# Optimization experiments

Measured on AMD Instinct MI355X. Metric: run time of the kernel, lower is better.

The kernel has to match this reference:

```python
import jax, jax.numpy as jnp
import numpy as np
import math

D_MODEL = 1024
NUM_HEADS = 16
HEAD_DIM = D_MODEL // NUM_HEADS
BATCH = 2
SEQ = 2048
THETA = 10000.0


def _rope_tables(seq_len, head_dim, theta=THETA):
    inv_freq = 1.0 / theta ** (jnp.arange(0, head_dim, 2, dtype=jnp.float32) / head_dim)
    pos = jnp.arange(seq_len, dtype=jnp.float32)
    freqs = jnp.outer(pos, inv_freq)                 # [S, hd/2]
    emb = jnp.concatenate([freqs, freqs], axis=-1)   # [S, hd]
    return jnp.cos(emb), jnp.sin(emb)


def _rotate_half(x):
    x1, x2 = jnp.split(x, 2, axis=-1)
    return jnp.concatenate([-x2, x1], axis=-1)


def setup_inputs() -> dict:
    key = jax.random.key(0)
    k1, k2, k3 = jax.random.split(key, 3)
    x = jax.random.normal(k1, (BATCH, SEQ, D_MODEL), dtype=jnp.float32)
    # causal mask: 1 where attend allowed, 0 where masked
    mask = jnp.tril(jnp.ones((SEQ, SEQ), dtype=jnp.int32))[None, None]
    w_qkv = jax.random.normal(k2, (D_MODEL, 3 * D_MODEL), dtype=jnp.float32) / math.sqrt(D_MODEL)
    w_out = jax.random.normal(k3, (D_MODEL, D_MODEL), dtype=jnp.float32) / math.sqrt(D_MODEL)
    return {"x": x, "mask": mask, "w_qkv": w_qkv, "w_out": w_out}


def reference(x, mask, w_qkv, w_out):
    B, S, _ = x.shape
    qkv = x @ w_qkv                                          # [B,S,3*D]
    qkv = qkv.reshape(B, S, 3, NUM_HEADS, HEAD_DIM)
    qkv = jnp.transpose(qkv, (2, 0, 3, 1, 4))                # [3,B,H,S,hd]
    q, k, v = qkv[0], qkv[1], qkv[2]
    cos, sin = _rope_tables(S, HEAD_DIM)                     # [S,hd]
    cos = cos[None, None]; sin = sin[None, None]
    q = q * cos + _rotate_half(q) * sin
    k = k * cos + _rotate_half(k) * sin
    scores = jnp.einsum('bhqd,bhkd->bhqk', q, k) / math.sqrt(HEAD_DIM)
    scores = jnp.where(mask == 0, -jnp.inf, scores)
    attn = jax.nn.softmax(scores, axis=-1)                   # dropout p=0 (eval)
    out = jnp.einsum('bhqk,bhkd->bhqd', attn, v)             # [B,H,S,hd]
    out = jnp.transpose(out, (0, 2, 1, 3)).reshape(B, S, D_MODEL)
    return out @ w_out
```

## Files before the change

### kernel.cpp

```cpp
#include <hip/hip_runtime.h>

typedef __bf16 bf16;
typedef __bf16 bf16x4 __attribute__((ext_vector_type(4)));
typedef __bf16 bf16x8 __attribute__((ext_vector_type(8)));
typedef float f32x4 __attribute__((ext_vector_type(4)));

constexpr int BATCH = 2;
constexpr int SEQ   = 2048;
constexpr int DMODEL= 1024;
constexpr int NH    = 16;
constexpr int HD    = 64;
constexpr int M_ROWS= BATCH * SEQ;
constexpr int N_QKV = 3 * DMODEL;

__device__ __forceinline__ void gl_lds16(const bf16* g, bf16* l) {
  __builtin_amdgcn_global_load_lds(
      (const __attribute__((address_space(1))) unsigned int*)g,
      (__attribute__((address_space(3))) unsigned int*)l, 16, 0, 0);
}

__global__ __launch_bounds__(256) void transpose_cast_kernel(
    const float* __restrict__ src, bf16* __restrict__ dst, int R, int C) {
  __shared__ float tile[32][33];
  const int c0 = blockIdx.x * 32, r0 = blockIdx.y * 32;
  const int tx = threadIdx.x, ty = threadIdx.y;
#pragma unroll
  for (int i = 0; i < 4; i++)
    tile[ty + 8 * i][tx] = src[(size_t)(r0 + ty + 8 * i) * C + c0 + tx];
  __syncthreads();
#pragma unroll
  for (int i = 0; i < 4; i++)
    dst[(size_t)(c0 + ty + 8 * i) * R + r0 + tx] = (bf16)tile[tx][ty + 8 * i];
}

__global__ __launch_bounds__(256) void cast_f32_bf16(
    const float* __restrict__ src, bf16* __restrict__ dst) {
  const int i = (blockIdx.x * 256 + threadIdx.x) * 8;
  float4 f0 = *(const float4*)&src[i];
  float4 f1 = *(const float4*)&src[i + 4];
  bf16x8 v;
  v[0] = (bf16)f0.x; v[1] = (bf16)f0.y; v[2] = (bf16)f0.z; v[3] = (bf16)f0.w;
  v[4] = (bf16)f1.x; v[5] = (bf16)f1.y; v[6] = (bf16)f1.z; v[7] = (bf16)f1.w;
  *(bf16x8*)&dst[i] = v;
}

#define GEMM_BODY(A, BT, K)                                                    \
  __shared__ bf16 As[128 * 32];                                                \
  __shared__ bf16 Bs[128 * 32];                                                \
  const int t = threadIdx.x;                                                   \
  const int m0 = blockIdx.y * 128;                                             \
  const int n0 = blockIdx.x * 128;                                             \
  const int w = t >> 6, lane = t & 63, g = lane >> 4, li = lane & 15;          \
  const int r0w = (w & 1) * 64, c0w = (w >> 1) * 64;                           \
  f32x4 acc[4][4] = {};                                                        \
  for (int k0 = 0; k0 < (K); k0 += 32) {                                       \
    __syncthreads();                                                           \
    _Pragma("unroll") for (int c = 0; c < 2; c++) {                            \
      const int idx = (w * 2 + c) * 64 + lane;                                 \
      const int row = idx >> 2, col = (idx & 3) * 8;                           \
      gl_lds16(&(A)[(size_t)(m0 + row) * (K) + k0 + col],                      \
               &As[(w * 2 + c) * 512]);                                        \
      gl_lds16(&(BT)[(size_t)(n0 + row) * (K) + k0 + col],                     \
               &Bs[(w * 2 + c) * 512]);                                        \
    }                                                                          \
    __syncthreads();                                                           \
    bf16x8 a[4], b[4];                                                         \
    _Pragma("unroll") for (int mt = 0; mt < 4; mt++)                           \
        a[mt] = *(const bf16x8*)&As[(r0w + mt * 16 + li) * 32 + g * 8];        \
    _Pragma("unroll") for (int nt = 0; nt < 4; nt++)                           \
        b[nt] = *(const bf16x8*)&Bs[(c0w + nt * 16 + li) * 32 + g * 8];        \
    _Pragma("unroll") for (int mt = 0; mt < 4; mt++)                           \
        _Pragma("unroll") for (int nt = 0; nt < 4; nt++)                       \
            acc[mt][nt] = __builtin_amdgcn_mfma_f32_16x16x32_bf16(             \
                a[mt], b[nt], acc[mt][nt], 0, 0, 0);                           \
  }

__global__ __launch_bounds__(256) void gemm_out(
    const bf16* __restrict__ A, const bf16* __restrict__ BT,
    float* __restrict__ C, int M, int N, int K) {
  GEMM_BODY(A, BT, K)
#pragma unroll
  for (int mt = 0; mt < 4; mt++)
#pragma unroll
    for (int nt = 0; nt < 4; nt++)
#pragma unroll
      for (int r = 0; r < 4; r++) {
        const int m = m0 + r0w + mt * 16 + g * 4 + r;
        const int n = n0 + c0w + nt * 16 + li;
        C[(size_t)m * N + n] = acc[mt][nt][r];
      }
}

__global__ __launch_bounds__(256) void gemm_qkv_rope(
    const bf16* __restrict__ A, const bf16* __restrict__ BT,
    bf16* __restrict__ Qb, bf16* __restrict__ Kb, bf16* __restrict__ Vt) {
  constexpr int K = DMODEL;
  GEMM_BODY(A, BT, K)

  const int region = n0 >> 10;
  const int b = m0 >> 11;
  const int h = ((n0 + c0w) >> 6) & 15;
  const size_t bh = (size_t)(b * NH + h);

  if (region < 2) {
    bf16* dst = region == 0 ? Qb : Kb;
    const float outsc = region == 0 ? 0.125f * 1.44269504f : 1.f;
    const float L = 13.287712379549449f;
    const float if0 = exp2f(-(float)(2 * li) / 64.f * L);
    const float if1 = exp2f(-(float)(2 * (li + 16)) / 64.f * L);
#pragma unroll
    for (int mt = 0; mt < 4; mt++)
#pragma unroll
      for (int r = 0; r < 4; r++) {
        const int s = (m0 + r0w + mt * 16 + g * 4 + r) & (SEQ - 1);
        float cs[2], sn[2];
        __sincosf((float)s * if0, &sn[0], &cs[0]);
        __sincosf((float)s * if1, &sn[1], &cs[1]);
#pragma unroll
        for (int nt = 0; nt < 4; nt++) {
          const int d = nt * 16 + li;
          const int par = nt & 1;
          const float a = acc[mt][nt][r];
          const float ap = acc[mt][nt ^ 2][r];
          const float v = (nt < 2) ? a * cs[par] - ap * sn[par]
                                   : a * cs[par] + ap * sn[par];
          dst[(bh * SEQ + s) * HD + d] = (bf16)(v * outsc);
        }
      }
  } else {
#pragma unroll
    for (int mt = 0; mt < 4; mt++)
#pragma unroll
      for (int nt = 0; nt < 4; nt++) {
        const int s = (m0 + r0w + mt * 16 + g * 4) & (SEQ - 1);
        const int d = nt * 16 + li;
        bf16x4 v;
#pragma unroll
        for (int r = 0; r < 4; r++) v[r] = (bf16)acc[mt][nt][r];
        *(bf16x4*)&Vt[(bh * HD + d) * SEQ + s] = v;
      }
  }
}

__global__ __launch_bounds__(256) void flash_attn4(
    const bf16* __restrict__ Q, const bf16* __restrict__ Kb,
    const bf16* __restrict__ Vt, bf16* __restrict__ Oout) {
  const int f = blockIdx.x;
  const int c = f & 255, half = f >> 8;
  const int bh = c >> 3, idx = c & 7;
  const int qt = half ? 15 - idx : idx;
  const int q0 = qt * 128;
  const int t = threadIdx.x, w = t >> 6, lane = t & 63, g = lane >> 4,
            li = lane & 15;

  __shared__ bf16 Ks[2][4096];
  __shared__ bf16 Vs[2][4096];
  __shared__ bf16 Pl[4][32][72];

  const bf16* Qh = Q  + (size_t)bh * SEQ * HD;
  const bf16* Kh = Kb + (size_t)bh * SEQ * HD;
  const bf16* Vh = Vt + (size_t)bh * HD * SEQ;

  const int qw = q0 + w * 32;

  bf16x8 qf[2][2];
#pragma unroll
  for (int mt = 0; mt < 2; mt++)
#pragma unroll
    for (int ks = 0; ks < 2; ks++)
      qf[mt][ks] =
          *(const bf16x8*)&Qh[(size_t)(qw + mt * 16 + li) * HD + ks * 32 + g * 8];

  f32x4 o[2][4] = {};
  float l_[2][4] = {};

  const int sp0 = (w * 2) * 64 + lane, sp1 = (w * 2 + 1) * 64 + lane;
  const int sr0 = sp0 >> 3, sc0 = ((sp0 & 7) ^ (sr0 & 7)) * 8;
  const int sr1 = sp1 >> 3, sc1 = ((sp1 & 7) ^ (sr1 & 7)) * 8;

  const int jend = q0 + 128;
  gl_lds16(&Kh[(size_t)sr0 * HD + sc0], &Ks[0][(w * 2) * 512]);
  gl_lds16(&Vh[(size_t)sr0 * SEQ + sc0], &Vs[0][(w * 2) * 512]);
  gl_lds16(&Kh[(size_t)sr1 * HD + sc1], &Ks[0][(w * 2 + 1) * 512]);
  gl_lds16(&Vh[(size_t)sr1 * SEQ + sc1], &Vs[0][(w * 2 + 1) * 512]);
  __syncthreads();

  for (int j0 = 0; j0 < jend; j0 += 64) {
    const int cur = (j0 >> 6) & 1, nxt = cur ^ 1;
    if (j0 + 64 < jend) {
      const int jn = j0 + 64;
      gl_lds16(&Kh[(size_t)(jn + sr0) * HD + sc0], &Ks[nxt][(w * 2) * 512]);
      gl_lds16(&Vh[(size_t)sr0 * SEQ + jn + sc0], &Vs[nxt][(w * 2) * 512]);
      gl_lds16(&Kh[(size_t)(jn + sr1) * HD + sc1], &Ks[nxt][(w * 2 + 1) * 512]);
      gl_lds16(&Vh[(size_t)sr1 * SEQ + jn + sc1], &Vs[nxt][(w * 2 + 1) * 512]);
    }

    if (j0 <= qw + 31) {
      f32x4 sacc[2][4] = {};
#pragma unroll
      for (int ks = 0; ks < 2; ks++)
#pragma unroll
        for (int nt = 0; nt < 4; nt++) {
          const int rK = nt * 16 + li;
          const int pK = rK * 8 + ((ks * 4 + g) ^ (li & 7));
          bf16x8 kf = *(const bf16x8*)&Ks[cur][pK * 8];
          sacc[0][nt] = __builtin_amdgcn_mfma_f32_16x16x32_bf16(
              qf[0][ks], kf, sacc[0][nt], 0, 0, 0);
          sacc[1][nt] = __builtin_amdgcn_mfma_f32_16x16x32_bf16(
              qf[1][ks], kf, sacc[1][nt], 0, 0, 0);
        }

      const bool masked = (j0 + 63 > qw);
#pragma unroll
      for (int mt = 0; mt < 2; mt++)
#pragma unroll
        for (int nt = 0; nt < 4; nt++)
#pragma unroll
          for (int r = 0; r < 4; r++) {
            float v = sacc[mt][nt][r];
            if (masked) {
              const int kc = j0 + nt * 16 + li;
              const int qr = qw + mt * 16 + g * 4 + r;
              v = (kc <= qr) ? v : -1e30f;
            }
            const float p = exp2f(v);
            l_[mt][r] += p;
            Pl[w][mt * 16 + g * 4 + r][nt * 16 + li] = (bf16)p;
          }

#pragma unroll
      for (int ks = 0; ks < 2; ks++) {
        bf16x8 pf0 = *(const bf16x8*)&Pl[w][li][ks * 32 + g * 8];
        bf16x8 pf1 = *(const bf16x8*)&Pl[w][16 + li][ks * 32 + g * 8];
#pragma unroll
        for (int dt = 0; dt < 4; dt++) {
          const int rV = dt * 16 + li;
          const int pV = rV * 8 + ((ks * 4 + g) ^ (li & 7));
          bf16x8 vf = *(const bf16x8*)&Vs[cur][pV * 8];
          o[0][dt] = __builtin_amdgcn_mfma_f32_16x16x32_bf16(pf0, vf, o[0][dt],
                                                             0, 0, 0);
          o[1][dt] = __builtin_amdgcn_mfma_f32_16x16x32_bf16(pf1, vf, o[1][dt],
                                                             0, 0, 0);
        }
      }
    }
    __syncthreads();
  }

#pragma unroll
  for (int off = 1; off < 16; off <<= 1)
#pragma unroll
    for (int mt = 0; mt < 2; mt++)
#pragma unroll
      for (int r = 0; r < 4; r++) l_[mt][r] += __shfl_xor(l_[mt][r], off, 64);

  const int b = bh >> 4, h = bh & 15;
#pragma unroll
  for (int mt = 0; mt < 2; mt++)
#pragma unroll
    for (int dt = 0; dt < 4; dt++)
#pragma unroll
      for (int r = 0; r < 4; r++) {
        const int s = qw + mt * 16 + g * 4 + r;
        const int d = dt * 16 + li;
        const float v = o[mt][dt][r] / l_[mt][r];
        Oout[((size_t)(b * SEQ + s)) * DMODEL + h * 64 + d] = (bf16)v;
      }
}

extern "C" void kernel_launch(void* const* d_in, const int* in_sizes, int n_in,
                              void* d_out, int out_size, void* d_ws,
                              size_t ws_size, hipStream_t stream) {
  const float* x     = (const float*)d_in[0];
  const float* w_qkv = (const float*)d_in[2];
  const float* w_out = (const float*)d_in[3];
  float* out = (float*)d_out;

  char* ws = (char*)d_ws;
  bf16* WqkvT = (bf16*)(ws);
  bf16* WoutT = (bf16*)(ws + 6291456);
  bf16* xb    = (bf16*)(ws + 8388608);
  bf16* Qb    = (bf16*)(ws + 16777216);
  bf16* Kbuf  = (bf16*)(ws + 25165824);
  bf16* Vt    = (bf16*)(ws + 33554432);
  bf16* attn  = (bf16*)(ws + 41943040);

  cast_f32_bf16<<<M_ROWS * DMODEL / 2048, 256, 0, stream>>>(x, xb);
  transpose_cast_kernel<<<dim3(N_QKV / 32, DMODEL / 32), dim3(32, 8), 0,
                          stream>>>(w_qkv, WqkvT, DMODEL, N_QKV);
  transpose_cast_kernel<<<dim3(DMODEL / 32, DMODEL / 32), dim3(32, 8), 0,
                          stream>>>(w_out, WoutT, DMODEL, DMODEL);
  gemm_qkv_rope<<<dim3(N_QKV / 128, M_ROWS / 128), 256, 0, stream>>>(
      xb, WqkvT, Qb, Kbuf, Vt);
  flash_attn4<<<dim3(512), 256, 0, stream>>>(Qb, Kbuf, Vt, attn);
  gemm_out<<<dim3(DMODEL / 128, M_ROWS / 128), 256, 0, stream>>>(
      attn, WoutT, out, M_ROWS, DMODEL, DMODEL);
}
```

Measured before the change: 228.6 us.

## Split flash attention across 8 waves with 16-row query tiles and causal tile skipping

The attention kernel now uses 512 threads (8 waves), and each wave owns 16 query rows instead of 32. The cooperative K/V loads become one load per thread per tile instead of two. In diagonal tiles, the QK MFMAs for fully masked 16-column sub-tiles are skipped and their P entries written as zero. The P scratch buffer moves to an XOR-swizzled layout to reduce LDS bank conflicts. This aims to raise wave-level parallelism and cut wasted causal work, at the cost of less Q-fragment reuse per K/V read and more barrier participants per block.

```diff
diff --git a/kernel.cpp b/kernel.cpp
--- a/kernel.cpp
+++ b/kernel.cpp
@@ -142,7 +142,7 @@
   }
 }
 
-__global__ __launch_bounds__(256) void flash_attn4(
+__global__ __launch_bounds__(512, 4) void flash_attn5(
     const bf16* __restrict__ Q, const bf16* __restrict__ Kb,
     const bf16* __restrict__ Vt, bf16* __restrict__ Oout) {
   const int f = blockIdx.x;
@@ -155,94 +155,91 @@
 
   __shared__ bf16 Ks[2][4096];
   __shared__ bf16 Vs[2][4096];
-  __shared__ bf16 Pl[4][32][72];
+  __shared__ bf16 Pl[8 * 1024];
 
   const bf16* Qh = Q  + (size_t)bh * SEQ * HD;
   const bf16* Kh = Kb + (size_t)bh * SEQ * HD;
   const bf16* Vh = Vt + (size_t)bh * HD * SEQ;
 
-  const int qw = q0 + w * 32;
-
-  bf16x8 qf[2][2];
-#pragma unroll
-  for (int mt = 0; mt < 2; mt++)
-#pragma unroll
-    for (int ks = 0; ks < 2; ks++)
-      qf[mt][ks] =
-          *(const bf16x8*)&Qh[(size_t)(qw + mt * 16 + li) * HD + ks * 32 + g * 8];
-
-  f32x4 o[2][4] = {};
-  float l_[2][4] = {};
-
-  const int sp0 = (w * 2) * 64 + lane, sp1 = (w * 2 + 1) * 64 + lane;
-  const int sr0 = sp0 >> 3, sc0 = ((sp0 & 7) ^ (sr0 & 7)) * 8;
-  const int sr1 = sp1 >> 3, sc1 = ((sp1 & 7) ^ (sr1 & 7)) * 8;
+  const int qw = q0 + w * 16;
+
+  bf16x8 qf[2];
+#pragma unroll
+  for (int ks = 0; ks < 2; ks++)
+    qf[ks] = *(const bf16x8*)&Qh[(size_t)(qw + li) * HD + ks * 32 + g * 8];
+
+  f32x4 o[4] = {};
+  float l_[4] = {};
+
+  const int p = w * 64 + lane;
+  const int sr = p >> 3, sc = ((p & 7) ^ (sr & 7)) * 8;
+  const int ldsoff = w * 512;
 
   const int jend = q0 + 128;
-  gl_lds16(&Kh[(size_t)sr0 * HD + sc0], &Ks[0][(w * 2) * 512]);
-  gl_lds16(&Vh[(size_t)sr0 * SEQ + sc0], &Vs[0][(w * 2) * 512]);
-  gl_lds16(&Kh[(size_t)sr1 * HD + sc1], &Ks[0][(w * 2 + 1) * 512]);
-  gl_lds16(&Vh[(size_t)sr1 * SEQ + sc1], &Vs[0][(w * 2 + 1) * 512]);
+  gl_lds16(&Kh[(size_t)sr * HD + sc], &Ks[0][ldsoff]);
+  gl_lds16(&Vh[(size_t)sr * SEQ + sc], &Vs[0][ldsoff]);
   __syncthreads();
 
   for (int j0 = 0; j0 < jend; j0 += 64) {
     const int cur = (j0 >> 6) & 1, nxt = cur ^ 1;
     if (j0 + 64 < jend) {
       const int jn = j0 + 64;
-      gl_lds16(&Kh[(size_t)(jn + sr0) * HD + sc0], &Ks[nxt][(w * 2) * 512]);
-      gl_lds16(&Vh[(size_t)sr0 * SEQ + jn + sc0], &Vs[nxt][(w * 2) * 512]);
-      gl_lds16(&Kh[(size_t)(jn + sr1) * HD + sc1], &Ks[nxt][(w * 2 + 1) * 512]);
-      gl_lds16(&Vh[(size_t)sr1 * SEQ + jn + sc1], &Vs[nxt][(w * 2 + 1) * 512]);
+      gl_lds16(&Kh[(size_t)(jn + sr) * HD + sc], &Ks[nxt][ldsoff]);
+      gl_lds16(&Vh[(size_t)sr * SEQ + jn + sc], &Vs[nxt][ldsoff]);
     }
 
-    if (j0 <= qw + 31) {
-      f32x4 sacc[2][4] = {};
+    if (j0 <= qw + 15) {
+      const bool masked = (j0 + 63 > qw);
+      const int ntlim = masked ? ((qw + 15 - j0) >> 4) + 1 : 4;
+
+      f32x4 sacc[4] = {};
 #pragma unroll
       for (int ks = 0; ks < 2; ks++)
 #pragma unroll
         for (int nt = 0; nt < 4; nt++) {
+          if (nt >= ntlim) continue;
           const int rK = nt * 16 + li;
           const int pK = rK * 8 + ((ks * 4 + g) ^ (li & 7));
           bf16x8 kf = *(const bf16x8*)&Ks[cur][pK * 8];
-          sacc[0][nt] = __builtin_amdgcn_mfma_f32_16x16x32_bf16(
-              qf[0][ks], kf, sacc[0][nt], 0, 0, 0);
-          sacc[1][nt] = __builtin_amdgcn_mfma_f32_16x16x32_bf16(
-              qf[1][ks], kf, sacc[1][nt], 0, 0, 0);
-        }
-
-      const bool masked = (j0 + 63 > qw);
-#pragma unroll
-      for (int mt = 0; mt < 2; mt++)
-#pragma unroll
-        for (int nt = 0; nt < 4; nt++)
-#pragma unroll
-          for (int r = 0; r < 4; r++) {
-            float v = sacc[mt][nt][r];
-            if (masked) {
-              const int kc = j0 + nt * 16 + li;
-              const int qr = qw + mt * 16 + g * 4 + r;
-              v = (kc <= qr) ? v : -1e30f;
-            }
-            const float p = exp2f(v);
-            l_[mt][r] += p;
-            Pl[w][mt * 16 + g * 4 + r][nt * 16 + li] = (bf16)p;
+          sacc[nt] = __builtin_amdgcn_mfma_f32_16x16x32_bf16(qf[ks], kf,
+                                                             sacc[nt], 0, 0, 0);
+        }
+
+#pragma unroll
+      for (int nt = 0; nt < 4; nt++)
+#pragma unroll
+        for (int r = 0; r < 4; r++) {
+          const int row = g * 4 + r, col = nt * 16 + li;
+          const int ch = row * 8 + ((col >> 3) ^ (row & 7));
+          bf16 pv;
+          if (nt < ntlim) {
+            float v = sacc[nt][r];
+            if (masked) v = (j0 + col <= qw + row) ? v : -1e30f;
+            const float pe = exp2f(v);
+            l_[r] += pe;
+            pv = (bf16)pe;
+          } else {
+            pv = (bf16)0.f;
           }
-
+          Pl[w * 1024 + ch * 8 + (col & 7)] = pv;
+        }
+
+      bf16x8 pf[2];
 #pragma unroll
       for (int ks = 0; ks < 2; ks++) {
-        bf16x8 pf0 = *(const bf16x8*)&Pl[w][li][ks * 32 + g * 8];
-        bf16x8 pf1 = *(const bf16x8*)&Pl[w][16 + li][ks * 32 + g * 8];
+        const int pP = li * 8 + ((ks * 4 + g) ^ (li & 7));
+        pf[ks] = *(const bf16x8*)&Pl[w * 1024 + pP * 8];
+      }
+#pragma unroll
+      for (int ks = 0; ks < 2; ks++)
 #pragma unroll
         for (int dt = 0; dt < 4; dt++) {
           const int rV = dt * 16 + li;
           const int pV = rV * 8 + ((ks * 4 + g) ^ (li & 7));
           bf16x8 vf = *(const bf16x8*)&Vs[cur][pV * 8];
-          o[0][dt] = __builtin_amdgcn_mfma_f32_16x16x32_bf16(pf0, vf, o[0][dt],
-                                                             0, 0, 0);
-          o[1][dt] = __builtin_amdgcn_mfma_f32_16x16x32_bf16(pf1, vf, o[1][dt],
-                                                             0, 0, 0);
-        }
-      }
+          o[dt] = __builtin_amdgcn_mfma_f32_16x16x32_bf16(pf[ks], vf, o[dt],
+                                                          0, 0, 0);
+        }
     }
     __syncthreads();
   }
@@ -250,22 +247,18 @@
 #pragma unroll
   for (int off = 1; off < 16; off <<= 1)
 #pragma unroll
-    for (int mt = 0; mt < 2; mt++)
-#pragma unroll
-      for (int r = 0; r < 4; r++) l_[mt][r] += __shfl_xor(l_[mt][r], off, 64);
+    for (int r = 0; r < 4; r++) l_[r] += __shfl_xor(l_[r], off, 64);
 
   const int b = bh >> 4, h = bh & 15;
 #pragma unroll
-  for (int mt = 0; mt < 2; mt++)
-#pragma unroll
-    for (int dt = 0; dt < 4; dt++)
-#pragma unroll
-      for (int r = 0; r < 4; r++) {
-        const int s = qw + mt * 16 + g * 4 + r;
-        const int d = dt * 16 + li;
-        const float v = o[mt][dt][r] / l_[mt][r];
-        Oout[((size_t)(b * SEQ + s)) * DMODEL + h * 64 + d] = (bf16)v;
-      }
+  for (int dt = 0; dt < 4; dt++)
+#pragma unroll
+    for (int r = 0; r < 4; r++) {
+      const int s = qw + g * 4 + r;
+      const int d = dt * 16 + li;
+      Oout[((size_t)(b * SEQ + s)) * DMODEL + h * 64 + d] =
+          (bf16)(o[dt][r] / l_[r]);
+    }
 }
 
 extern "C" void kernel_launch(void* const* d_in, const int* in_sizes, int n_in,
@@ -292,7 +285,7 @@
                           stream>>>(w_out, WoutT, DMODEL, DMODEL);
   gemm_qkv_rope<<<dim3(N_QKV / 128, M_ROWS / 128), 256, 0, stream>>>(
       xb, WqkvT, Qb, Kbuf, Vt);
-  flash_attn4<<<dim3(512), 256, 0, stream>>>(Qb, Kbuf, Vt, attn);
+  flash_attn5<<<dim3(512), 512, 0, stream>>>(Qb, Kbuf, Vt, attn);
   gemm_out<<<dim3(DMODEL / 128, M_ROWS / 128), 256, 0, stream>>>(
       attn, WoutT, out, M_ROWS, DMODEL, DMODEL);
 }
```

Result: no change. 230.0 us (+0.6%).
